# Kernel optimization log

Hardware: AMD Instinct MI355X
Metric: run time of the kernel (lower is better)

## Reference

```python
import jax, jax.numpy as jnp
import numpy as np

N = 50000        # nodes
E = 800000       # edges
FEAT = 64        # cfg.feature_dim
HID = 128        # cfg.hidden_dim
G = 8            # num graphs
EPS = 1e-5       # LayerNorm eps
MIN_DEPTH, MAX_DEPTH = 0.1, 3.0


def _ln(x, g, b):
    m = jnp.mean(x, axis=-1, keepdims=True)
    v = jnp.mean((x - m) ** 2, axis=-1, keepdims=True)
    return (x - m) * jax.lax.rsqrt(v + EPS) * g + b


def setup_inputs() -> dict:
    key = jax.random.key(0)
    ks = jax.random.split(key, 32)
    f32 = jnp.float32
    inp = {}
    inp['x'] = jax.random.normal(ks[0], (N, FEAT), dtype=f32)
    inp['edge_index'] = jax.random.randint(ks[1], (2, E), 0, N)
    inp['batch'] = jnp.sort(jax.random.randint(ks[2], (N,), 0, G))
    # input_projection: Linear(FEAT,HID) + LayerNorm
    inp['in_w'] = jax.random.normal(ks[3], (FEAT, HID), dtype=f32) * (1.0 / np.sqrt(FEAT))
    inp['in_b'] = jnp.zeros((HID,), f32)
    inp['in_ln_g'] = jnp.ones((HID,), f32)
    inp['in_ln_b'] = jnp.zeros((HID,), f32)
    # epigenetics
    inp['methylation'] = jnp.zeros((HID,), f32)
    inp['histones'] = jnp.zeros((4,), f32)
    inp['log_depth'] = jnp.zeros((), f32)
    # NeuralODEFunc: 3 stacked GCNConv(HID,HID) + LayerNorms, gate MLP, residual scalar
    inp['gcn_w'] = jax.random.normal(ks[4], (3, HID, HID), dtype=f32) * (1.0 / np.sqrt(HID))
    inp['gcn_b'] = jnp.zeros((3, HID), f32)
    inp['ln_g'] = jnp.ones((3, HID), f32)
    inp['ln_b'] = jnp.zeros((3, HID), f32)
    inp['gate_w'] = jax.random.normal(ks[5], (2 * HID, HID), dtype=f32) * (1.0 / np.sqrt(2 * HID))
    inp['gate_b'] = jnp.zeros((HID,), f32)
    inp['residual_weight'] = jnp.asarray(0.1, f32)
    # output_projection: Linear(HID,HID) + LayerNorm
    inp['out_w'] = jax.random.normal(ks[6], (HID, HID), dtype=f32) * (1.0 / np.sqrt(HID))
    inp['out_b'] = jnp.zeros((HID,), f32)
    inp['out_ln_g'] = jnp.ones((HID,), f32)
    inp['out_ln_b'] = jnp.zeros((HID,), f32)
    return inp


def reference(x, edge_index, batch, in_w, in_b, in_ln_g, in_ln_b, methylation,
              histones, log_depth, gcn_w, gcn_b, ln_g, ln_b, gate_w, gate_b,
              residual_weight, out_w, out_b, out_ln_g, out_ln_b):
    n = x.shape[0]
    src, dst = edge_index[0], edge_index[1]

    # input_projection (Dropout is identity in eval)
    h = jax.nn.relu(_ln(x @ in_w + in_b, in_ln_g, in_ln_b))

    # epigenetic regulation (chromatin_accessibility goes through .item() -> constant)
    meth_sil = jnp.mean(jax.nn.sigmoid(methylation))
    hm = jax.nn.sigmoid(histones)
    act = (hm[0] + hm[2]) * 0.5
    rep = (hm[1] + hm[3]) * 0.5
    chrom = jax.lax.stop_gradient(jnp.clip(act - rep + 0.5, 0.0, 1.0))
    h = h * (chrom * (1.0 - meth_sil))

    # symmetric GCN normalization, no self loops (computed once, no grad path)
    deg = jax.ops.segment_sum(jnp.ones((E,), h.dtype), dst, num_segments=n)
    dinv = jnp.where(deg > 0, jax.lax.rsqrt(jnp.maximum(deg, 1.0)), 0.0)
    enorm = (dinv[src] * dinv[dst])[:, None]  # [E,1]

    def gcn(hh, i):
        xw = hh @ gcn_w[i]                                   # [N,H]
        agg = jax.ops.segment_sum(xw[src] * enorm, dst, num_segments=n)
        return agg + gcn_b[i]

    def ode_f(hh):
        h_orig = hh
        cur = hh
        for i in range(3):  # fixed layer count
            h_new = _ln(gcn(cur, i), ln_g[i], ln_b[i])
            if i > 0:
                gate = jax.nn.sigmoid(
                    jnp.concatenate([cur, h_new], axis=-1) @ gate_w + gate_b)
                cur = gate * h_new + (1.0 - gate) * cur
            else:
                cur = h_new
        cur = jnp.tanh(cur)
        return cur + residual_weight * h_orig

    # depth via .item() in torch -> non-differentiable constant
    depth = jax.lax.stop_gradient(
        jnp.clip(jnp.exp(log_depth), MIN_DEPTH, MAX_DEPTH))
    # single fixed RK4 step over t = linspace(0, depth, 2)
    dt = depth
    k1 = ode_f(h)
    k2 = ode_f(h + 0.5 * dt * k1)
    k3 = ode_f(h + 0.5 * dt * k2)
    k4 = ode_f(h + dt * k3)
    h_final = h + (dt / 6.0) * (k1 + 2.0 * k2 + 2.0 * k3 + k4)

    # output_projection + global_mean_pool over batch
    h_out = _ln(h_final @ out_w + out_b, out_ln_g, out_ln_b)
    cnt = jax.ops.segment_sum(jnp.ones((n,), h.dtype), batch, num_segments=G)
    pooled = jax.ops.segment_sum(h_out, batch, num_segments=G)
    return pooled / jnp.maximum(cnt, 1.0)[:, None]
```

## Files before the change

### kernel.cpp

```cpp
#include <hip/hip_runtime.h>
#include <math.h>

#define NN 50000
#define EE 800000
#define HH 128
#define FF 64
#define GG 8
#define PB 500
#define SB 1600

using short8 = __attribute__((ext_vector_type(8))) short;
using f32x4  = __attribute__((ext_vector_type(4))) float;
using f32x2  = __attribute__((ext_vector_type(2))) float;

__device__ __forceinline__ float sigm(float x){ return 1.0f/(1.0f+expf(-x)); }
__device__ __forceinline__ unsigned short f2bf(float f){
    union { float f; unsigned u; } v; v.f = f;
    unsigned r = v.u + 0x7fff + ((v.u >> 16) & 1);
    return (unsigned short)(r >> 16);
}
__device__ __forceinline__ float bf2f(unsigned short h){
    union { unsigned u; float f; } v; v.u = ((unsigned)h) << 16;
    return v.f;
}

#if __has_builtin(__builtin_amdgcn_cvt_pk_fp8_f32) && __has_builtin(__builtin_amdgcn_cvt_pk_f32_fp8)
#define FP8_HW 1
#else
#define FP8_HW 0
#endif

__device__ __forceinline__ unsigned fp8enc1_sw(float f){
    union { float fl; unsigned u; } x; x.fl = f;
    unsigned s = (x.u >> 31) << 7;
    float a = fabsf(f);
    if (!(a > 0.f)) return s;
    if (a >= 448.f) return s | 0x7E;
    if (a < 0.015625f) {
        int q = (int)(a * 512.f + 0.5f);
        if (q > 7) return s | (1u << 3);
        return s | (unsigned)q;
    }
    unsigned u = x.u + (1u << 19);
    int e32 = (int)((u >> 23) & 255) - 127;
    if (e32 < -6) { int q=(int)(a*512.f+0.5f); if(q>7)q=7; return s|(unsigned)q; }
    if (e32 > 8) return s | 0x7E;
    unsigned m = (u >> 20) & 7;
    return s | ((unsigned)(e32 + 7) << 3) | m;
}
__device__ __forceinline__ float fp8dec1_sw(unsigned v){
    unsigned s = v >> 7, e = (v >> 3) & 15, m = v & 7;
    float f;
    if (e == 0) f = (float)m * 0.001953125f;
    else { union { unsigned u; float fl; } x; x.u = ((e + 120u) << 23) | (m << 20); f = x.fl; }
    return s ? -f : f;
}
__device__ __forceinline__ unsigned char e2fp8(float a){
#if FP8_HW
    return (unsigned char)(__builtin_amdgcn_cvt_pk_fp8_f32(a, a, 0, false) & 0xFF);
#else
    return (unsigned char)fp8enc1_sw(a);
#endif
}
__device__ __forceinline__ float2 d2fp8(unsigned short u){
#if FP8_HW
    f32x2 r = __builtin_amdgcn_cvt_pk_f32_fp8((int)(unsigned)u, false);
    return make_float2(r[0], r[1]);
#else
    return make_float2(fp8dec1_sw(u & 0xFF), fp8dec1_sw((u >> 8) & 0xFF));
#endif
}

__global__ void k_setup(const float* __restrict__ meth,
                        const float* __restrict__ histones,
                        const float* __restrict__ logd,
                        float* __restrict__ scal,
                        const int* __restrict__ batch, int* __restrict__ st)
{
    if (blockIdx.x == 1) {
        int g = threadIdx.x;
        if (g > GG) return;
        int lo = 0, hi = NN;
        while (lo < hi) { int mid = (lo + hi) >> 1; if (batch[mid] < g) lo = mid + 1; else hi = mid; }
        st[g] = lo;
        return;
    }
    int l = threadIdx.x;
    float s = sigm(meth[l]) + sigm(meth[l + 64]);
#pragma unroll
    for (int o = 32; o >= 1; o >>= 1) s += __shfl_xor(s, o, 64);
    if (l == 0) {
        float msil = s * (1.0f / 128.0f);
        float h0 = sigm(histones[0]), h1 = sigm(histones[1]);
        float h2 = sigm(histones[2]), h3 = sigm(histones[3]);
        float act = (h0 + h2) * 0.5f, rep = (h1 + h3) * 0.5f;
        float chrom = fminf(fmaxf(act - rep + 0.5f, 0.0f), 1.0f);
        scal[0] = chrom * (1.0f - msil);
        float d = expf(logd[0]);
        scal[1] = fminf(fmaxf(d, 0.1f), 3.0f);
    }
}

__global__ void k_packall(const float* __restrict__ in_w, const float* __restrict__ gcn_w,
                          const float* __restrict__ gate_w, const float* __restrict__ out_w,
                          unsigned short* __restrict__ outp)
{
    int i = blockIdx.x * 256 + threadIdx.x;
    if (i >= 8192 + 6 * 16384) return;
    const float* src; int base, li;
    if (i < 8192) { src = in_w + i; base = 0; li = i; }
    else {
        int j = i - 8192;
        int m = j >> 14, r = j & 16383;
        base = 8192 + (m << 14); li = r;
        if (m < 3)      src = gcn_w  + m * 16384 + r;
        else if (m < 5) src = gate_w + (m - 3) * 16384 + r;
        else            src = out_w + r;
    }
    int k = li >> 7, n = li & 127;
    int c = k >> 5, kl = k & 31, q = kl >> 3, j2 = kl & 7;
    int b = n >> 4, ln = n & 15;
    int lane = q * 16 + ln;
    outp[base + ((c * 8 + b) * 64 + lane) * 8 + j2] = f2bf(*src);
}

__global__ void k_cvtx(const float* __restrict__ x, unsigned short* __restrict__ xb)
{
    size_t i = (size_t)blockIdx.x * 256 + threadIdx.x;
    if (i >= (size_t)NN * 16) return;
    float4 v = ((const float4*)x)[i];
    ushort4 o;
    o.x = f2bf(v.x); o.y = f2bf(v.y); o.z = f2bf(v.z); o.w = f2bf(v.w);
    ((ushort4*)xb)[i] = o;
}

__global__ void k_hist(const int* __restrict__ ei, int* __restrict__ hist)
{
    int e = blockIdx.x * 256 + threadIdx.x;
    if (e < EE) atomicAdd(&hist[ei[EE + e]], 1);
}

__global__ void k_dinv(const int* __restrict__ hist, float* __restrict__ dinv)
{
    int n = blockIdx.x * 256 + threadIdx.x;
    if (n < NN) {
        int d = hist[n];
        dinv[n] = d > 0 ? rsqrtf((float)d) : 0.0f;
    }
}

__global__ void k_scan_a(const int* __restrict__ hist, int* __restrict__ aux)
{
    __shared__ int sh[256];
    int b = blockIdx.x, t = threadIdx.x;
    int base = b * 1024 + t * 4;
    int s = 0;
#pragma unroll
    for (int j = 0; j < 4; ++j) { int i = base + j; if (i < NN) s += hist[i]; }
    sh[t] = s; __syncthreads();
    for (int o = 128; o >= 1; o >>= 1) { if (t < o) sh[t] += sh[t + o]; __syncthreads(); }
    if (t == 0) aux[b] = sh[0];
}

__global__ void k_scan_b(int* __restrict__ aux, int nb)
{
    if (blockIdx.x == 0 && threadIdx.x == 0) {
        int run = 0;
        for (int i = 0; i < nb; ++i) { int v = aux[i]; aux[i] = run; run += v; }
    }
}

__global__ void k_scan_c(const int* __restrict__ hist, const int* __restrict__ aux,
                         int* __restrict__ row_ptr, int* __restrict__ cursor)
{
    __shared__ int sh[256];
    int b = blockIdx.x, t = threadIdx.x;
    int base = b * 1024 + t * 4;
    int v[4]; int s = 0;
#pragma unroll
    for (int j = 0; j < 4; ++j) { int i = base + j; v[j] = (i < NN) ? hist[i] : 0; s += v[j]; }
    sh[t] = s; __syncthreads();
    for (int o = 1; o < 256; o <<= 1) {
        int x = 0; if (t >= o) x = sh[t - o];
        __syncthreads(); sh[t] += x; __syncthreads();
    }
    int run = aux[b] + sh[t] - s;
#pragma unroll
    for (int j = 0; j < 4; ++j) {
        int i = base + j;
        if (i < NN) { row_ptr[i] = run; cursor[i] = run; }
        run += v[j];
    }
    if (b == 0 && t == 0) { row_ptr[NN] = EE; cursor[NN] = EE; }
}

__global__ __launch_bounds__(256) void k_scatter(const int* __restrict__ ei,
                          int* __restrict__ cursor, unsigned* __restrict__ ew)
{
    if (blockIdx.x == 0 && threadIdx.x < 128)
        ew[EE + threadIdx.x] = 0u;
    const int grp = blockIdx.x & 7;
    const int blk = blockIdx.x >> 3;
    const int CH  = EE / (SB / 8);
    const int e0 = blk * CH, e1 = e0 + CH;
    const int glo = grp * (NN / 8), ghi = glo + (NN / 8);
    for (int e = e0 + threadIdx.x; e < e1; e += 256) {
        int d = __builtin_nontemporal_load(ei + EE + e);
        if (d >= glo && d < ghi) {
            int s = __builtin_nontemporal_load(ei + e);
            int p = atomicAdd(&cursor[d], 1);
            ew[p] = (unsigned)s | ((unsigned)(d & 15) << 16);
        }
    }
}

template<int KC, int MODE>
__global__ __launch_bounds__(256) void k_dense_mfma(
    const unsigned short* __restrict__ A, const unsigned short* __restrict__ Wp,
    const float* __restrict__ bias, const float* __restrict__ lng,
    const float* __restrict__ lnb, const float* __restrict__ scal,
    const float* __restrict__ dinv,
    unsigned short* __restrict__ out, unsigned char* __restrict__ out8)
{
    __shared__ unsigned short Ws[KC * 4096];
    const int t = threadIdx.x;
    {
        const float4* src = (const float4*)Wp;
        float4* dst = (float4*)Ws;
#pragma unroll
        for (int i = 0; i < KC * 2; ++i) dst[t + i * 256] = src[t + i * 256];
    }
    __syncthreads();
    const int wave = t >> 6, lane = t & 63;
    const int quad = lane >> 4, ln = lane & 15;
    const int r0 = blockIdx.x * 64 + wave * 16;
    const int K = KC * 32;
    const int arow = r0 + ln;
    const bool av = arow < NN;

    f32x4 acc[8] = {};
#pragma unroll
    for (int c = 0; c < KC; ++c) {
        short8 a = {};
        if (av) a = *(const short8*)(A + (size_t)arow * K + c * 32 + quad * 8);
#pragma unroll
        for (int b = 0; b < 8; ++b) {
            short8 bb = *(const short8*)&Ws[((c * 8 + b) * 64 + lane) * 8];
            acc[b] = __builtin_amdgcn_mfma_f32_16x16x32_bf16(a, bb, acc[b], 0, 0, 0);
        }
    }

    float b_s[8], g_s[8], e_s[8];
#pragma unroll
    for (int b = 0; b < 8; ++b) {
        int col = b * 16 + ln;
        b_s[b] = bias[col]; g_s[b] = lng[col]; e_s[b] = lnb[col];
    }
    float sc = (MODE == 1) ? scal[0] : 0.0f;
#pragma unroll
    for (int i = 0; i < 4; ++i) {
        int row = r0 + quad * 4 + i;
        float v[8]; float s = 0.f, q = 0.f;
#pragma unroll
        for (int b = 0; b < 8; ++b) { float x = acc[b][i] + b_s[b]; v[b] = x; s += x; q += x * x; }
#pragma unroll
        for (int o = 1; o < 16; o <<= 1) { s += __shfl_xor(s, o, 64); q += __shfl_xor(q, o, 64); }
        float m  = s * (1.0f / 128.0f);
        float vr = q * (1.0f / 128.0f) - m * m;
        float rs = rsqrtf(vr + 1e-5f);
        if (row < NN) {
            float dv = out8 ? dinv[row] : 0.f;
#pragma unroll
            for (int b = 0; b < 8; ++b) {
                float o2 = (v[b] - m) * rs * g_s[b] + e_s[b];
                if (MODE == 1) o2 = fmaxf(o2, 0.f) * sc;
                out[(size_t)row * 128 + b * 16 + ln] = f2bf(o2);
                if (out8) out8[(size_t)row * 128 + b * 16 + ln] = e2fp8(o2 * dv);
            }
        }
    }
}

__global__ __launch_bounds__(128) void k_spgemm(
    const int* __restrict__ rp, const unsigned* __restrict__ ew,
    const unsigned char* __restrict__ X8, const unsigned short* __restrict__ Wp,
    const float* __restrict__ bias, const float* __restrict__ lng,
    const float* __restrict__ lnb, const float* __restrict__ dinv,
    unsigned short* __restrict__ out, unsigned char* __restrict__ out8)
{
    __shared__ float accf[2][16 * 132];
    const int t = threadIdx.x, wave = t >> 6, lane = t & 63;
    const int quad = lane >> 4, ln = lane & 15;
    const int half = lane >> 5, li = lane & 31;
    const int n0 = blockIdx.x * 16;
    const int nf = n0 + wave * 8;

    {
        float* z0 = &accf[0][wave * 8 * 132];
        float* z1 = &accf[1][wave * 8 * 132];
        for (int i = lane; i < 8 * 132; i += 64) { z0[i] = 0.f; z1[i] = 0.f; }
    }

    if (nf < NN) {
        const int nl = min(nf + 8, NN);
        const int ebeg = __builtin_amdgcn_readfirstlane(rp[nf]);
        const int eend = __builtin_amdgcn_readfirstlane(rp[nl]);
        if (ebeg < eend) {
            float4 racc = make_float4(0.f, 0.f, 0.f, 0.f);
            int curd = (int)((ew[min(ebeg + half, eend - 1)] >> 16) & 15u);
            const unsigned char* Xl = X8 + li * 4;
            unsigned rec[8], recN[8], g[8];
#pragma unroll
            for (int j = 0; j < 8; ++j) rec[j]  = ew[ebeg + 2 * j + half];
#pragma unroll
            for (int j = 0; j < 8; ++j) recN[j] = ew[ebeg + 16 + 2 * j + half];
#pragma unroll
            for (int j = 0; j < 8; ++j) {
                int src = (int)(rec[j] & 0xFFFFu);
                g[j] = *(const unsigned*)(Xl + (size_t)src * 128);
            }
            for (int e = ebeg; e < eend; e += 16) {
                unsigned gN[8], recNN[8];
#pragma unroll
                for (int j = 0; j < 8; ++j) {
                    int src = (int)(recN[j] & 0xFFFFu);
                    gN[j] = *(const unsigned*)(Xl + (size_t)src * 128);
                }
#pragma unroll
                for (int j = 0; j < 8; ++j) recNN[j] = ew[e + 32 + 2 * j + half];
                int lim = eend - e;
                int mj = lim > half ? ((lim - half + 1) >> 1) : 0; if (mj > 8) mj = 8;
#pragma unroll
                for (int j = 0; j < 8; ++j) {
                    if (j >= mj) break;
                    int dl = (int)((rec[j] >> 16) & 15u);
                    if (dl != curd) {
                        *(float4*)&accf[half][curd * 132 + li * 4] = racc;
                        racc = make_float4(0.f, 0.f, 0.f, 0.f);
                        curd = dl;
                    }
                    float2 p0 = d2fp8((unsigned short)(g[j] & 0xFFFFu));
                    float2 p1 = d2fp8((unsigned short)(g[j] >> 16));
                    racc.x += p0.x;
                    racc.y += p0.y;
                    racc.z += p1.x;
                    racc.w += p1.y;
                }
#pragma unroll
                for (int j = 0; j < 8; ++j) { rec[j] = recN[j]; recN[j] = recNN[j]; g[j] = gN[j]; }
            }
            *(float4*)&accf[half][curd * 132 + li * 4] = racc;
        }
    }
    __syncthreads();

    f32x4 acc[8] = {};
    const float* ar0 = &accf[0][(size_t)ln * 132];
    const float* ar1 = &accf[1][(size_t)ln * 132];
#pragma unroll
    for (int c = 0; c < 4; ++c) {
        float4 a0 = *(const float4*)(ar0 + c * 32 + quad * 8);
        float4 a1 = *(const float4*)(ar0 + c * 32 + quad * 8 + 4);
        float4 b0 = *(const float4*)(ar1 + c * 32 + quad * 8);
        float4 b1 = *(const float4*)(ar1 + c * 32 + quad * 8 + 4);
        short8 af;
        af[0] = (short)f2bf(a0.x + b0.x); af[1] = (short)f2bf(a0.y + b0.y);
        af[2] = (short)f2bf(a0.z + b0.z); af[3] = (short)f2bf(a0.w + b0.w);
        af[4] = (short)f2bf(a1.x + b1.x); af[5] = (short)f2bf(a1.y + b1.y);
        af[6] = (short)f2bf(a1.z + b1.z); af[7] = (short)f2bf(a1.w + b1.w);
#pragma unroll
        for (int b = 0; b < 8; ++b) {
            short8 bb = *(const short8*)(Wp + ((size_t)(c * 8 + b) * 64 + lane) * 8);
            acc[b] = __builtin_amdgcn_mfma_f32_16x16x32_bf16(af, bb, acc[b], 0, 0, 0);
        }
    }

    float b_s[8], g_s[8], e_s[8];
#pragma unroll
    for (int b = 0; b < 8; ++b) {
        int col = b * 16 + ln;
        b_s[b] = bias[col]; g_s[b] = lng[col]; e_s[b] = lnb[col];
    }
#pragma unroll
    for (int i = 0; i < 4; ++i) {
        int row = n0 + quad * 4 + i;
        float dv = (row < NN) ? dinv[row] : 0.f;
        float v[8]; float s = 0.f, q = 0.f;
#pragma unroll
        for (int b = 0; b < 8; ++b) { float x = acc[b][i] * dv + b_s[b]; v[b] = x; s += x; q += x * x; }
#pragma unroll
        for (int o = 1; o < 16; o <<= 1) { s += __shfl_xor(s, o, 64); q += __shfl_xor(q, o, 64); }
        float m  = s * (1.0f / 128.0f);
        float vr = q * (1.0f / 128.0f) - m * m;
        float rs = rsqrtf(vr + 1e-5f);
        if (((quad >> 1) == wave) && row < NN) {
#pragma unroll
            for (int b = 0; b < 8; ++b) {
                float o2 = (v[b] - m) * rs * g_s[b] + e_s[b];
                out[(size_t)row * 128 + b * 16 + ln] = f2bf(o2);
                if (out8) out8[(size_t)row * 128 + b * 16 + ln] = e2fp8(o2 * dv);
            }
        }
    }
}

__global__ __launch_bounds__(256) void k_gate_mfma(
    unsigned short* __restrict__ cur, const unsigned short* __restrict__ hnew,
    const unsigned short* __restrict__ Wp, const float* __restrict__ gb,
    const float* __restrict__ dinv, unsigned char* __restrict__ cur8)
{
    __shared__ unsigned short Ws[16384];
    const int t = threadIdx.x;
    const int wave = t >> 6, lane = t & 63;
    const int quad = lane >> 4, ln = lane & 15;
    const int r0 = blockIdx.x * 64 + wave * 16;
    const int arow = r0 + ln;
    const bool av = arow < NN;

    f32x4 acc[8] = {};
#pragma unroll
    for (int s = 0; s < 2; ++s) {
        __syncthreads();
        {
            const float4* src = (const float4*)(Wp + (size_t)s * 16384);
            float4* dst = (float4*)Ws;
#pragma unroll
            for (int i = 0; i < 8; ++i) dst[t + i * 256] = src[t + i * 256];
        }
        __syncthreads();
        const unsigned short* A = s ? hnew : cur;
#pragma unroll
        for (int c = 0; c < 4; ++c) {
            short8 a = {};
            if (av) a = *(const short8*)(A + (size_t)arow * 128 + c * 32 + quad * 8);
#pragma unroll
            for (int b = 0; b < 8; ++b) {
                short8 bb = *(const short8*)&Ws[((c * 8 + b) * 64 + lane) * 8];
                acc[b] = __builtin_amdgcn_mfma_f32_16x16x32_bf16(a, bb, acc[b], 0, 0, 0);
            }
        }
    }

    float gb_s[8];
#pragma unroll
    for (int b = 0; b < 8; ++b) gb_s[b] = gb[b * 16 + ln];
#pragma unroll
    for (int i = 0; i < 4; ++i) {
        int row = r0 + quad * 4 + i;
        if (row < NN) {
            float dv = dinv[row];
#pragma unroll
            for (int b = 0; b < 8; ++b) {
                size_t idx = (size_t)row * 128 + b * 16 + ln;
                float g  = sigm(acc[b][i] + gb_s[b]);
                float cu = bf2f(cur[idx]);
                float hn = bf2f(hnew[idx]);
                float r  = g * hn + (1.f - g) * cu;
                cur[idx]  = f2bf(r);
                cur8[idx] = e2fp8(r * dv);
            }
        }
    }
}

template<int S>
__global__ __launch_bounds__(256) void k_gate_fused(
    const unsigned short* __restrict__ cur, const unsigned short* __restrict__ hnew,
    const unsigned short* __restrict__ Wp, const float* __restrict__ gb,
    const unsigned short* __restrict__ fin, const unsigned short* __restrict__ h0,
    unsigned short* __restrict__ tv1, unsigned short* __restrict__ tv2,
    unsigned short* __restrict__ tv3,
    unsigned short* __restrict__ ybuf, unsigned char* __restrict__ y8,
    const float* __restrict__ scal, const float* __restrict__ rwp,
    const float* __restrict__ dinv)
{
    __shared__ unsigned short Ws[16384];
    const int t = threadIdx.x;
    const int wave = t >> 6, lane = t & 63;
    const int quad = lane >> 4, ln = lane & 15;
    const int r0 = blockIdx.x * 64 + wave * 16;
    const int arow = r0 + ln;
    const bool av = arow < NN;

    f32x4 am[8] = {};
#pragma unroll
    for (int s = 0; s < 2; ++s) {
        __syncthreads();
        {
            const float4* src = (const float4*)(Wp + (size_t)s * 16384);
            float4* dst = (float4*)Ws;
#pragma unroll
            for (int i = 0; i < 8; ++i) dst[t + i * 256] = src[t + i * 256];
        }
        __syncthreads();
        const unsigned short* A = s ? hnew : cur;
#pragma unroll
        for (int c = 0; c < 4; ++c) {
            short8 a = {};
            if (av) a = *(const short8*)(A + (size_t)arow * 128 + c * 32 + quad * 8);
#pragma unroll
            for (int b = 0; b < 8; ++b) {
                short8 bb = *(const short8*)&Ws[((c * 8 + b) * 64 + lane) * 8];
                am[b] = __builtin_amdgcn_mfma_f32_16x16x32_bf16(a, bb, am[b], 0, 0, 0);
            }
        }
    }

    float gb_s[8];
#pragma unroll
    for (int b = 0; b < 8; ++b) gb_s[b] = gb[b * 16 + ln];
    const float dt = scal[1], rw = rwp[0];
    const float cn = (S == 3) ? dt : 0.5f * dt;
    const float w16 = dt * (1.f / 6.f), w13 = dt * (1.f / 3.f);
#pragma unroll
    for (int i = 0; i < 4; ++i) {
        int row = r0 + quad * 4 + i;
        if (row < NN) {
            float dv = dinv[row];
#pragma unroll
            for (int b = 0; b < 8; ++b) {
                size_t idx = (size_t)row * 128 + b * 16 + ln;
                float g  = sigm(am[b][i] + gb_s[b]);
                float cu = bf2f(cur[idx]);
                float hn = bf2f(hnew[idx]);
                float r  = g * hn + (1.f - g) * cu;
                float tv = tanhf(r) + rw * bf2f(fin[idx]);
                float yv;
                if (S == 4) {
                    float t1 = bf2f(tv1[idx]);
                    float t2 = bf2f(tv2[idx]);
                    float t3 = bf2f(tv3[idx]);
                    yv = bf2f(h0[idx]) + w16 * (t1 + tv) + w13 * (t2 + t3);
                } else {
                    if (S == 1) tv1[idx] = f2bf(tv);
                    if (S == 2) tv2[idx] = f2bf(tv);
                    if (S == 3) tv3[idx] = f2bf(tv);
                    yv = bf2f(h0[idx]) + cn * tv;
                }
                ybuf[idx] = f2bf(yv);
                if (S != 4) y8[idx] = e2fp8(yv * dv);
            }
        }
    }
}

__global__ __launch_bounds__(128) void k_pool1(
    const unsigned short* __restrict__ h, const int* __restrict__ batch,
    float* __restrict__ partial)
{
    int c = threadIdx.x, b = blockIdx.x;
    int r0 = b * (NN / PB), r1 = r0 + (NN / PB);
    float acc = 0.f;
    int gfirst = batch[r0], g = gfirst;
#pragma unroll 4
    for (int r = r0; r < r1; ++r) {
        int gg = batch[r];
        if (gg != g) {
            partial[(size_t)b * 1024 + g * 128 + c] = acc;
            for (int z = g + 1; z < gg; ++z) partial[(size_t)b * 1024 + z * 128 + c] = 0.f;
            acc = 0.f; g = gg;
        }
        acc += bf2f(h[(size_t)r * 128 + c]);
    }
    partial[(size_t)b * 1024 + g * 128 + c] = acc;
    for (int z = 0; z < gfirst; ++z)  partial[(size_t)b * 1024 + z * 128 + c] = 0.f;
    for (int z = g + 1; z < GG; ++z)  partial[(size_t)b * 1024 + z * 128 + c] = 0.f;
}

__global__ __launch_bounds__(256) void k_pool2(
    const float* __restrict__ partial, const int* __restrict__ st,
    float* __restrict__ out)
{
    __shared__ float sh[8][32];
    int cb = blockIdx.x & 3, g = blockIdx.x >> 2;
    int cl = threadIdx.x & 31, sl = threadIdx.x >> 5;
    int c = cb * 32 + cl;
    float s = 0.f;
    for (int b = sl; b < PB; b += 8) s += partial[(size_t)b * 1024 + g * 128 + c];
    sh[sl][cl] = s; __syncthreads();
    if (sl == 0) {
        float tt = 0.f;
#pragma unroll
        for (int i = 0; i < 8; ++i) tt += sh[i][cl];
        int cnt = st[g + 1] - st[g];
        out[g * 128 + c] = tt / (float)(cnt > 0 ? cnt : 1);
    }
}

static inline size_t al(size_t x) { return (x + 255) & ~(size_t)255; }

extern "C" void kernel_launch(void* const* d_in, const int* in_sizes, int n_in,
                              void* d_out, int out_size, void* d_ws, size_t ws_size,
                              hipStream_t stream)
{
    const float* x       = (const float*)d_in[0];
    const int*   ei      = (const int*)d_in[1];
    const int*   batch   = (const int*)d_in[2];
    const float* in_w    = (const float*)d_in[3];
    const float* in_b    = (const float*)d_in[4];
    const float* in_lng  = (const float*)d_in[5];
    const float* in_lnb  = (const float*)d_in[6];
    const float* meth    = (const float*)d_in[7];
    const float* histn   = (const float*)d_in[8];
    const float* logd    = (const float*)d_in[9];
    const float* gcn_w   = (const float*)d_in[10];
    const float* gcn_b   = (const float*)d_in[11];
    const float* ln_g    = (const float*)d_in[12];
    const float* ln_b    = (const float*)d_in[13];
    const float* gate_w  = (const float*)d_in[14];
    const float* gate_b  = (const float*)d_in[15];
    const float* rw      = (const float*)d_in[16];
    const float* out_w   = (const float*)d_in[17];
    const float* out_b   = (const float*)d_in[18];
    const float* out_lng = (const float*)d_in[19];
    const float* out_lnb = (const float*)d_in[20];
    float* out = (float*)d_out;

    char* w = (char*)d_ws;
    size_t off = 0;
    float* scal   = (float*)(w + off); off += al(16 * 4);
    int*   hist   = (int*)(w + off);   off += al((size_t)NN * 4);
    int*   rp     = (int*)(w + off);   off += al((size_t)(NN + 1) * 4);
    int*   cursor = (int*)(w + off);   off += al((size_t)(NN + 1) * 4);
    int*   aux    = (int*)(w + off);   off += al(64 * 4);
    int*   st     = (int*)(w + off);   off += al(16 * 4);
    float* dinv   = (float*)(w + off); off += al((size_t)NN * 4);
    unsigned* ew  = (unsigned*)(w + off); off += al((size_t)(EE + 128) * 4);
    float* partial= (float*)(w + off); off += al((size_t)PB * 1024 * 4);
    unsigned short* wpak = (unsigned short*)(w + off); off += al((size_t)(8192 + 6 * 16384) * 2);
    unsigned short* inwp  = wpak;
    unsigned short* gcnwp = wpak + 8192;
    unsigned short* gwp   = wpak + 8192 + 3 * 16384;
    unsigned short* owp   = wpak + 8192 + 5 * 16384;
    size_t B16 = al((size_t)NN * 128 * 2);
    unsigned short* xb  = (unsigned short*)(w + off); off += al((size_t)NN * 64 * 2);
    unsigned short* h0  = (unsigned short*)(w + off); off += B16;
    unsigned short* y   = (unsigned short*)(w + off); off += B16;
    unsigned short* cur = (unsigned short*)(w + off); off += B16;
    unsigned short* t2  = (unsigned short*)(w + off); off += B16;
    unsigned short* tv1 = (unsigned short*)(w + off); off += B16;
    unsigned short* tv2 = (unsigned short*)(w + off); off += B16;
    unsigned short* tv3 = (unsigned short*)(w + off); off += B16;
    size_t B8 = al((size_t)NN * 128);
    unsigned char* h08  = (unsigned char*)(w + off); off += B8;
    unsigned char* y8   = (unsigned char*)(w + off); off += B8;
    unsigned char* cur8 = (unsigned char*)(w + off); off += B8;
    if (off > ws_size) return;

    hipMemsetAsync(hist, 0, (size_t)NN * 4, stream);

    k_setup<<<2, 64, 0, stream>>>(meth, histn, logd, scal, batch, st);
    k_packall<<<(8192 + 6 * 16384 + 255) / 256, 256, 0, stream>>>(in_w, gcn_w, gate_w, out_w, wpak);
    k_cvtx<<<3125, 256, 0, stream>>>(x, xb);

    k_hist<<<(EE + 255) / 256, 256, 0, stream>>>(ei, hist);
    k_dinv<<<(NN + 255) / 256, 256, 0, stream>>>(hist, dinv);
    k_scan_a<<<49, 256, 0, stream>>>(hist, aux);
    k_scan_b<<<1, 1, 0, stream>>>(aux, 49);
    k_scan_c<<<49, 256, 0, stream>>>(hist, aux, rp, cursor);
    k_scatter<<<SB, 256, 0, stream>>>(ei, cursor, ew);

    const int DG = (NN + 63) / 64;
    const int SG = (NN + 15) / 16;
    k_dense_mfma<2, 1><<<DG, 256, 0, stream>>>(xb, inwp, in_b, in_lng, in_lnb, scal, dinv, h0, h08);

    for (int s = 1; s <= 4; ++s) {
        const unsigned short* fin = (s == 1) ? h0 : y;
        const unsigned char*  fin8 = (s == 1) ? h08 : y8;
        k_spgemm<<<SG, 128, 0, stream>>>(rp, ew, fin8, gcnwp, gcn_b, ln_g, ln_b, dinv, cur, cur8);
        k_spgemm<<<SG, 128, 0, stream>>>(rp, ew, cur8,
                                         gcnwp + (size_t)1 * 128 * 128, gcn_b + 128,
                                         ln_g + 128, ln_b + 128, dinv, t2, (unsigned char*)0);
        k_gate_mfma<<<DG, 256, 0, stream>>>(cur, t2, gwp, gate_b, dinv, cur8);
        k_spgemm<<<SG, 128, 0, stream>>>(rp, ew, cur8,
                                         gcnwp + (size_t)2 * 128 * 128, gcn_b + 256,
                                         ln_g + 256, ln_b + 256, dinv, t2, (unsigned char*)0);
        if (s == 1)      k_gate_fused<1><<<DG, 256, 0, stream>>>(cur, t2, gwp, gate_b, fin, h0, tv1, tv2, tv3, y, y8, scal, rw, dinv);
        else if (s == 2) k_gate_fused<2><<<DG, 256, 0, stream>>>(cur, t2, gwp, gate_b, fin, h0, tv1, tv2, tv3, y, y8, scal, rw, dinv);
        else if (s == 3) k_gate_fused<3><<<DG, 256, 0, stream>>>(cur, t2, gwp, gate_b, fin, h0, tv1, tv2, tv3, y, y8, scal, rw, dinv);
        else             k_gate_fused<4><<<DG, 256, 0, stream>>>(cur, t2, gwp, gate_b, fin, h0, tv1, tv2, tv3, y, y8, scal, rw, dinv);
    }

    k_dense_mfma<4, 0><<<DG, 256, 0, stream>>>(y, owp, out_b, out_lng, out_lnb, scal, dinv, t2, (unsigned char*)0);
    k_pool1<<<PB, 128, 0, stream>>>(t2, batch, partial);
    k_pool2<<<GG * 4, 256, 0, stream>>>(partial, st, out);
}
```

Measured before the change: 845.5 us.

## Fuse gate MLP and RK4 epilogues into sparse GCN kernel

The separate gate kernels (k_gate_mfma, k_gate_fused) are folded into the spgemm kernel as templated epilogues. The LayerNorm output is staged in shared memory and the 256x128 gate GEMM runs directly on it, followed by the gating blend and the RK4 accumulation. This removes two kernel launches per ODE evaluation and a round trip through global memory for the new hidden state. In exchange the gate weights are read from global memory per block with no LDS staging, register pressure in spgemm rises, and the NN bounds checks are dropped on the assumption that NN divides evenly by 16.

```diff
diff --git a/kernel.cpp b/kernel.cpp
--- a/kernel.cpp
+++ b/kernel.cpp
@@ -281,11 +281,18 @@
     }
 }
 
+template<int EPI>
 __global__ __launch_bounds__(128) void k_spgemm(
     const int* __restrict__ rp, const unsigned* __restrict__ ew,
     const unsigned char* __restrict__ X8, const unsigned short* __restrict__ Wp,
     const float* __restrict__ bias, const float* __restrict__ lng,
     const float* __restrict__ lnb, const float* __restrict__ dinv,
+    const unsigned short* __restrict__ Gw, const float* __restrict__ gb,
+    const unsigned short* __restrict__ curg,
+    const unsigned short* __restrict__ fin, const unsigned short* __restrict__ h0,
+    unsigned short* __restrict__ tv1, unsigned short* __restrict__ tv2,
+    unsigned short* __restrict__ tv3,
+    const float* __restrict__ scal, const float* __restrict__ rwp,
     unsigned short* __restrict__ out, unsigned char* __restrict__ out8)
 {
     __shared__ float accf[2][16 * 132];
@@ -301,7 +308,7 @@
         for (int i = lane; i < 8 * 132; i += 64) { z0[i] = 0.f; z1[i] = 0.f; }
     }
 
-    if (nf < NN) {
+    {
         const int nl = min(nf + 8, NN);
         const int ebeg = __builtin_amdgcn_readfirstlane(rp[nf]);
         const int eend = __builtin_amdgcn_readfirstlane(rp[nl]);
@@ -355,23 +362,25 @@
     __syncthreads();
 
     f32x4 acc[8] = {};
-    const float* ar0 = &accf[0][(size_t)ln * 132];
-    const float* ar1 = &accf[1][(size_t)ln * 132];
-#pragma unroll
-    for (int c = 0; c < 4; ++c) {
-        float4 a0 = *(const float4*)(ar0 + c * 32 + quad * 8);
-        float4 a1 = *(const float4*)(ar0 + c * 32 + quad * 8 + 4);
-        float4 b0 = *(const float4*)(ar1 + c * 32 + quad * 8);
-        float4 b1 = *(const float4*)(ar1 + c * 32 + quad * 8 + 4);
-        short8 af;
-        af[0] = (short)f2bf(a0.x + b0.x); af[1] = (short)f2bf(a0.y + b0.y);
-        af[2] = (short)f2bf(a0.z + b0.z); af[3] = (short)f2bf(a0.w + b0.w);
-        af[4] = (short)f2bf(a1.x + b1.x); af[5] = (short)f2bf(a1.y + b1.y);
-        af[6] = (short)f2bf(a1.z + b1.z); af[7] = (short)f2bf(a1.w + b1.w);
-#pragma unroll
-        for (int b = 0; b < 8; ++b) {
-            short8 bb = *(const short8*)(Wp + ((size_t)(c * 8 + b) * 64 + lane) * 8);
-            acc[b] = __builtin_amdgcn_mfma_f32_16x16x32_bf16(af, bb, acc[b], 0, 0, 0);
+    {
+        const float* ar0 = &accf[0][(size_t)ln * 132];
+        const float* ar1 = &accf[1][(size_t)ln * 132];
+#pragma unroll
+        for (int c = 0; c < 4; ++c) {
+            float4 a0 = *(const float4*)(ar0 + c * 32 + quad * 8);
+            float4 a1 = *(const float4*)(ar0 + c * 32 + quad * 8 + 4);
+            float4 b0 = *(const float4*)(ar1 + c * 32 + quad * 8);
+            float4 b1 = *(const float4*)(ar1 + c * 32 + quad * 8 + 4);
+            short8 af;
+            af[0] = (short)f2bf(a0.x + b0.x); af[1] = (short)f2bf(a0.y + b0.y);
+            af[2] = (short)f2bf(a0.z + b0.z); af[3] = (short)f2bf(a0.w + b0.w);
+            af[4] = (short)f2bf(a1.x + b1.x); af[5] = (short)f2bf(a1.y + b1.y);
+            af[6] = (short)f2bf(a1.z + b1.z); af[7] = (short)f2bf(a1.w + b1.w);
+#pragma unroll
+            for (int b = 0; b < 8; ++b) {
+                short8 bb = *(const short8*)(Wp + ((size_t)(c * 8 + b) * 64 + lane) * 8);
+                acc[b] = __builtin_amdgcn_mfma_f32_16x16x32_bf16(af, bb, acc[b], 0, 0, 0);
+            }
         }
     }
 
@@ -381,164 +390,107 @@
         int col = b * 16 + ln;
         b_s[b] = bias[col]; g_s[b] = lng[col]; e_s[b] = lnb[col];
     }
-#pragma unroll
-    for (int i = 0; i < 4; ++i) {
-        int row = n0 + quad * 4 + i;
-        float dv = (row < NN) ? dinv[row] : 0.f;
-        float v[8]; float s = 0.f, q = 0.f;
-#pragma unroll
-        for (int b = 0; b < 8; ++b) { float x = acc[b][i] * dv + b_s[b]; v[b] = x; s += x; q += x * x; }
-#pragma unroll
-        for (int o = 1; o < 16; o <<= 1) { s += __shfl_xor(s, o, 64); q += __shfl_xor(q, o, 64); }
-        float m  = s * (1.0f / 128.0f);
-        float vr = q * (1.0f / 128.0f) - m * m;
-        float rs = rsqrtf(vr + 1e-5f);
-        if (((quad >> 1) == wave) && row < NN) {
+
+    if (EPI == 0) {
+#pragma unroll
+        for (int i = 0; i < 4; ++i) {
+            int row = n0 + quad * 4 + i;
+            float dv = dinv[row];
+            float v[8]; float s = 0.f, q = 0.f;
+#pragma unroll
+            for (int b = 0; b < 8; ++b) { float x = acc[b][i] * dv + b_s[b]; v[b] = x; s += x; q += x * x; }
+#pragma unroll
+            for (int o = 1; o < 16; o <<= 1) { s += __shfl_xor(s, o, 64); q += __shfl_xor(q, o, 64); }
+            float m  = s * (1.0f / 128.0f);
+            float vr = q * (1.0f / 128.0f) - m * m;
+            float rs = rsqrtf(vr + 1e-5f);
+            if ((quad >> 1) == wave) {
+#pragma unroll
+                for (int b = 0; b < 8; ++b) {
+                    float o2 = (v[b] - m) * rs * g_s[b] + e_s[b];
+                    out[(size_t)row * 128 + b * 16 + ln] = f2bf(o2);
+                    if (out8) out8[(size_t)row * 128 + b * 16 + ln] = e2fp8(o2 * dv);
+                }
+            }
+        }
+    } else {
+        __syncthreads();
+        unsigned short* hsh = (unsigned short*)&accf[0][0];
+#pragma unroll
+        for (int i = 0; i < 4; ++i) {
+            int rt = quad * 4 + i;
+            int row = n0 + rt;
+            float dv = dinv[row];
+            float v[8]; float s = 0.f, q = 0.f;
+#pragma unroll
+            for (int b = 0; b < 8; ++b) { float x = acc[b][i] * dv + b_s[b]; v[b] = x; s += x; q += x * x; }
+#pragma unroll
+            for (int o = 1; o < 16; o <<= 1) { s += __shfl_xor(s, o, 64); q += __shfl_xor(q, o, 64); }
+            float m  = s * (1.0f / 128.0f);
+            float vr = q * (1.0f / 128.0f) - m * m;
+            float rs = rsqrtf(vr + 1e-5f);
+            if ((quad >> 1) == wave) {
+#pragma unroll
+                for (int b = 0; b < 8; ++b)
+                    hsh[rt * 132 + b * 16 + ln] = f2bf((v[b] - m) * rs * g_s[b] + e_s[b]);
+            }
+        }
+        __syncthreads();
+
+        f32x4 gacc[8] = {};
+#pragma unroll
+        for (int c = 0; c < 4; ++c) {
+            short8 ac = *(const short8*)(curg + (size_t)(n0 + ln) * 128 + c * 32 + quad * 8);
+            short8 ah = *(const short8*)&hsh[ln * 132 + c * 32 + quad * 8];
 #pragma unroll
             for (int b = 0; b < 8; ++b) {
-                float o2 = (v[b] - m) * rs * g_s[b] + e_s[b];
-                out[(size_t)row * 128 + b * 16 + ln] = f2bf(o2);
-                if (out8) out8[(size_t)row * 128 + b * 16 + ln] = e2fp8(o2 * dv);
-            }
-        }
-    }
-}
-
-__global__ __launch_bounds__(256) void k_gate_mfma(
-    unsigned short* __restrict__ cur, const unsigned short* __restrict__ hnew,
-    const unsigned short* __restrict__ Wp, const float* __restrict__ gb,
-    const float* __restrict__ dinv, unsigned char* __restrict__ cur8)
-{
-    __shared__ unsigned short Ws[16384];
-    const int t = threadIdx.x;
-    const int wave = t >> 6, lane = t & 63;
-    const int quad = lane >> 4, ln = lane & 15;
-    const int r0 = blockIdx.x * 64 + wave * 16;
-    const int arow = r0 + ln;
-    const bool av = arow < NN;
-
-    f32x4 acc[8] = {};
-#pragma unroll
-    for (int s = 0; s < 2; ++s) {
-        __syncthreads();
-        {
-            const float4* src = (const float4*)(Wp + (size_t)s * 16384);
-            float4* dst = (float4*)Ws;
-#pragma unroll
-            for (int i = 0; i < 8; ++i) dst[t + i * 256] = src[t + i * 256];
-        }
-        __syncthreads();
-        const unsigned short* A = s ? hnew : cur;
-#pragma unroll
-        for (int c = 0; c < 4; ++c) {
-            short8 a = {};
-            if (av) a = *(const short8*)(A + (size_t)arow * 128 + c * 32 + quad * 8);
-#pragma unroll
-            for (int b = 0; b < 8; ++b) {
-                short8 bb = *(const short8*)&Ws[((c * 8 + b) * 64 + lane) * 8];
-                acc[b] = __builtin_amdgcn_mfma_f32_16x16x32_bf16(a, bb, acc[b], 0, 0, 0);
-            }
-        }
-    }
-
-    float gb_s[8];
-#pragma unroll
-    for (int b = 0; b < 8; ++b) gb_s[b] = gb[b * 16 + ln];
-#pragma unroll
-    for (int i = 0; i < 4; ++i) {
-        int row = r0 + quad * 4 + i;
-        if (row < NN) {
-            float dv = dinv[row];
-#pragma unroll
-            for (int b = 0; b < 8; ++b) {
-                size_t idx = (size_t)row * 128 + b * 16 + ln;
-                float g  = sigm(acc[b][i] + gb_s[b]);
-                float cu = bf2f(cur[idx]);
-                float hn = bf2f(hnew[idx]);
-                float r  = g * hn + (1.f - g) * cu;
-                cur[idx]  = f2bf(r);
-                cur8[idx] = e2fp8(r * dv);
-            }
-        }
-    }
-}
-
-template<int S>
-__global__ __launch_bounds__(256) void k_gate_fused(
-    const unsigned short* __restrict__ cur, const unsigned short* __restrict__ hnew,
-    const unsigned short* __restrict__ Wp, const float* __restrict__ gb,
-    const unsigned short* __restrict__ fin, const unsigned short* __restrict__ h0,
-    unsigned short* __restrict__ tv1, unsigned short* __restrict__ tv2,
-    unsigned short* __restrict__ tv3,
-    unsigned short* __restrict__ ybuf, unsigned char* __restrict__ y8,
-    const float* __restrict__ scal, const float* __restrict__ rwp,
-    const float* __restrict__ dinv)
-{
-    __shared__ unsigned short Ws[16384];
-    const int t = threadIdx.x;
-    const int wave = t >> 6, lane = t & 63;
-    const int quad = lane >> 4, ln = lane & 15;
-    const int r0 = blockIdx.x * 64 + wave * 16;
-    const int arow = r0 + ln;
-    const bool av = arow < NN;
-
-    f32x4 am[8] = {};
-#pragma unroll
-    for (int s = 0; s < 2; ++s) {
-        __syncthreads();
-        {
-            const float4* src = (const float4*)(Wp + (size_t)s * 16384);
-            float4* dst = (float4*)Ws;
-#pragma unroll
-            for (int i = 0; i < 8; ++i) dst[t + i * 256] = src[t + i * 256];
-        }
-        __syncthreads();
-        const unsigned short* A = s ? hnew : cur;
-#pragma unroll
-        for (int c = 0; c < 4; ++c) {
-            short8 a = {};
-            if (av) a = *(const short8*)(A + (size_t)arow * 128 + c * 32 + quad * 8);
-#pragma unroll
-            for (int b = 0; b < 8; ++b) {
-                short8 bb = *(const short8*)&Ws[((c * 8 + b) * 64 + lane) * 8];
-                am[b] = __builtin_amdgcn_mfma_f32_16x16x32_bf16(a, bb, am[b], 0, 0, 0);
-            }
-        }
-    }
-
-    float gb_s[8];
-#pragma unroll
-    for (int b = 0; b < 8; ++b) gb_s[b] = gb[b * 16 + ln];
-    const float dt = scal[1], rw = rwp[0];
-    const float cn = (S == 3) ? dt : 0.5f * dt;
-    const float w16 = dt * (1.f / 6.f), w13 = dt * (1.f / 3.f);
-#pragma unroll
-    for (int i = 0; i < 4; ++i) {
-        int row = r0 + quad * 4 + i;
-        if (row < NN) {
-            float dv = dinv[row];
-#pragma unroll
-            for (int b = 0; b < 8; ++b) {
-                size_t idx = (size_t)row * 128 + b * 16 + ln;
-                float g  = sigm(am[b][i] + gb_s[b]);
-                float cu = bf2f(cur[idx]);
-                float hn = bf2f(hnew[idx]);
-                float r  = g * hn + (1.f - g) * cu;
-                float tv = tanhf(r) + rw * bf2f(fin[idx]);
-                float yv;
-                if (S == 4) {
-                    float t1 = bf2f(tv1[idx]);
-                    float t2 = bf2f(tv2[idx]);
-                    float t3 = bf2f(tv3[idx]);
-                    yv = bf2f(h0[idx]) + w16 * (t1 + tv) + w13 * (t2 + t3);
-                } else {
-                    if (S == 1) tv1[idx] = f2bf(tv);
-                    if (S == 2) tv2[idx] = f2bf(tv);
-                    if (S == 3) tv3[idx] = f2bf(tv);
-                    yv = bf2f(h0[idx]) + cn * tv;
+                short8 w0 = *(const short8*)(Gw + ((size_t)(c * 8 + b) * 64 + lane) * 8);
+                short8 w1 = *(const short8*)(Gw + 16384 + ((size_t)(c * 8 + b) * 64 + lane) * 8);
+                gacc[b] = __builtin_amdgcn_mfma_f32_16x16x32_bf16(ac, w0, gacc[b], 0, 0, 0);
+                gacc[b] = __builtin_amdgcn_mfma_f32_16x16x32_bf16(ah, w1, gacc[b], 0, 0, 0);
+            }
+        }
+
+        float gb_s[8];
+#pragma unroll
+        for (int b = 0; b < 8; ++b) gb_s[b] = gb[b * 16 + ln];
+        float dt = 0.f, rw = 0.f;
+        if (EPI >= 2) { dt = scal[1]; rw = rwp[0]; }
+        const float cn  = (EPI == 4) ? dt : 0.5f * dt;
+        const float w16 = dt * (1.f / 6.f), w13 = dt * (1.f / 3.f);
+
+#pragma unroll
+        for (int i = 0; i < 4; ++i) {
+            int rt = quad * 4 + i;
+            int row = n0 + rt;
+            if ((quad >> 1) == wave) {
+                float dv = dinv[row];
+#pragma unroll
+                for (int b = 0; b < 8; ++b) {
+                    size_t idx = (size_t)row * 128 + b * 16 + ln;
+                    float hn = bf2f(hsh[rt * 132 + b * 16 + ln]);
+                    float g  = sigm(gacc[b][i] + gb_s[b]);
+                    float cu = bf2f(curg[idx]);
+                    float r  = g * hn + (1.f - g) * cu;
+                    if (EPI == 1) {
+                        out[idx]  = f2bf(r);
+                        out8[idx] = e2fp8(r * dv);
+                    } else {
+                        float tv = tanhf(r) + rw * bf2f(fin[idx]);
+                        float yv;
+                        if (EPI == 5) {
+                            yv = bf2f(h0[idx]) + w16 * (bf2f(tv1[idx]) + tv)
+                                               + w13 * (bf2f(tv2[idx]) + bf2f(tv3[idx]));
+                        } else {
+                            if (EPI == 2) tv1[idx] = f2bf(tv);
+                            if (EPI == 3) tv2[idx] = f2bf(tv);
+                            if (EPI == 4) tv3[idx] = f2bf(tv);
+                            yv = bf2f(h0[idx]) + cn * tv;
+                        }
+                        out[idx] = f2bf(yv);
+                        if (EPI != 5) out8[idx] = e2fp8(yv * dv);
+                    }
                 }
-                ybuf[idx] = f2bf(yv);
-                if (S != 4) y8[idx] = e2fp8(yv * dv);
             }
         }
     }
@@ -645,6 +597,7 @@
     unsigned char* h08  = (unsigned char*)(w + off); off += B8;
     unsigned char* y8   = (unsigned char*)(w + off); off += B8;
     unsigned char* cur8 = (unsigned char*)(w + off); off += B8;
+    unsigned char* t28  = (unsigned char*)(w + off); off += B8;
     if (off > ws_size) return;
 
     hipMemsetAsync(hist, 0, (size_t)NN * 4, stream);
@@ -667,18 +620,35 @@
     for (int s = 1; s <= 4; ++s) {
         const unsigned short* fin = (s == 1) ? h0 : y;
         const unsigned char*  fin8 = (s == 1) ? h08 : y8;
-        k_spgemm<<<SG, 128, 0, stream>>>(rp, ew, fin8, gcnwp, gcn_b, ln_g, ln_b, dinv, cur, cur8);
-        k_spgemm<<<SG, 128, 0, stream>>>(rp, ew, cur8,
-                                         gcnwp + (size_t)1 * 128 * 128, gcn_b + 128,
-                                         ln_g + 128, ln_b + 128, dinv, t2, (unsigned char*)0);
-        k_gate_mfma<<<DG, 256, 0, stream>>>(cur, t2, gwp, gate_b, dinv, cur8);
-        k_spgemm<<<SG, 128, 0, stream>>>(rp, ew, cur8,
-                                         gcnwp + (size_t)2 * 128 * 128, gcn_b + 256,
-                                         ln_g + 256, ln_b + 256, dinv, t2, (unsigned char*)0);
-        if (s == 1)      k_gate_fused<1><<<DG, 256, 0, stream>>>(cur, t2, gwp, gate_b, fin, h0, tv1, tv2, tv3, y, y8, scal, rw, dinv);
-        else if (s == 2) k_gate_fused<2><<<DG, 256, 0, stream>>>(cur, t2, gwp, gate_b, fin, h0, tv1, tv2, tv3, y, y8, scal, rw, dinv);
-        else if (s == 3) k_gate_fused<3><<<DG, 256, 0, stream>>>(cur, t2, gwp, gate_b, fin, h0, tv1, tv2, tv3, y, y8, scal, rw, dinv);
-        else             k_gate_fused<4><<<DG, 256, 0, stream>>>(cur, t2, gwp, gate_b, fin, h0, tv1, tv2, tv3, y, y8, scal, rw, dinv);
+        k_spgemm<0><<<SG, 128, 0, stream>>>(rp, ew, fin8, gcnwp, gcn_b, ln_g, ln_b, dinv,
+                                            (const unsigned short*)0, (const float*)0,
+                                            (const unsigned short*)0, (const unsigned short*)0,
+                                            (const unsigned short*)0, (unsigned short*)0,
+                                            (unsigned short*)0, (unsigned short*)0,
+                                            (const float*)0, (const float*)0, cur, cur8);
+        k_spgemm<1><<<SG, 128, 0, stream>>>(rp, ew, cur8,
+                                            gcnwp + (size_t)1 * 128 * 128, gcn_b + 128,
+                                            ln_g + 128, ln_b + 128, dinv,
+                                            gwp, gate_b, cur,
+                                            (const unsigned short*)0, (const unsigned short*)0,
+                                            (unsigned short*)0, (unsigned short*)0, (unsigned short*)0,
+                                            (const float*)0, (const float*)0, t2, t28);
+        if (s == 1)
+            k_spgemm<2><<<SG, 128, 0, stream>>>(rp, ew, t28,
+                gcnwp + (size_t)2 * 128 * 128, gcn_b + 256, ln_g + 256, ln_b + 256, dinv,
+                gwp, gate_b, t2, fin, h0, tv1, tv2, tv3, scal, rw, y, y8);
+        else if (s == 2)
+            k_spgemm<3><<<SG, 128, 0, stream>>>(rp, ew, t28,
+                gcnwp + (size_t)2 * 128 * 128, gcn_b + 256, ln_g + 256, ln_b + 256, dinv,
+                gwp, gate_b, t2, fin, h0, tv1, tv2, tv3, scal, rw, y, y8);
+        else if (s == 3)
+            k_spgemm<4><<<SG, 128, 0, stream>>>(rp, ew, t28,
+                gcnwp + (size_t)2 * 128 * 128, gcn_b + 256, ln_g + 256, ln_b + 256, dinv,
+                gwp, gate_b, t2, fin, h0, tv1, tv2, tv3, scal, rw, y, y8);
+        else
+            k_spgemm<5><<<SG, 128, 0, stream>>>(rp, ew, t28,
+                gcnwp + (size_t)2 * 128 * 128, gcn_b + 256, ln_g + 256, ln_b + 256, dinv,
+                gwp, gate_b, t2, fin, h0, tv1, tv2, tv3, scal, rw, y, y8);
     }
 
     k_dense_mfma<4, 0><<<DG, 256, 0, stream>>>(y, owp, out_b, out_lng, out_lnb, scal, dinv, t2, (unsigned char*)0);
```

New measurement: 1.075 ms. 1.27x slower.
